# Optimization experiments

Hardware: AMD Instinct MI355X
Metric: run time of the kernel (lower is better)

Reference implementation:

```python
import jax, jax.numpy as jnp
import numpy as np

N = 50000
E = 800000
D = 128
LN_EPS = 1e-5


def setup_inputs() -> dict:
    key = jax.random.key(0)
    ks = jax.random.split(key, 12)
    s = 1.0 / np.sqrt(D)
    return {
        "x": jax.random.normal(ks[0], (N, D), dtype=jnp.float32),
        "edge_index": jax.random.randint(ks[1], (2, E), 0, N, dtype=jnp.int64),
        "edge_attr": jax.random.normal(ks[2], (E, D), dtype=jnp.float32),
        # GINEConv edge projection Linear(edge_dim=D, in_channels=D)
        "Wl": jax.random.uniform(ks[3], (D, D), jnp.float32, -s, s),
        "bl": jax.random.uniform(ks[4], (D,), jnp.float32, -s, s),
        # mlp: Linear(D,D) -> ReLU -> Linear(D,D)
        "W1": jax.random.uniform(ks[5], (D, D), jnp.float32, -s, s),
        "b1": jax.random.uniform(ks[6], (D,), jnp.float32, -s, s),
        "W2": jax.random.uniform(ks[7], (D, D), jnp.float32, -s, s),
        "b2": jax.random.uniform(ks[8], (D,), jnp.float32, -s, s),
        # PyG LayerNorm affine
        "ln_w": jnp.ones((D,), jnp.float32),
        "ln_b": jnp.zeros((D,), jnp.float32),
    }


def reference(x, edge_index, edge_attr, Wl, bl, W1, b1, W2, b2, ln_w, ln_b):
    src = edge_index[0]  # j (message source)
    dst = edge_index[1]  # i (aggregation target)
    # GINEConv message: ReLU(x_j + lin(edge_attr)) -- gather + elementwise
    e = edge_attr @ Wl + bl                      # [E, D]
    msg = jax.nn.relu(x[src] + e)                # [E, D]
    # scatter-sum aggregation into destination nodes
    agg = jax.ops.segment_sum(msg, dst, num_segments=N)  # [N, D]
    # eps = 0 (train_eps=False): nn((1+eps)*x + agg)
    h = x + agg
    h = jax.nn.relu(h @ W1 + b1) @ W2 + b2       # MLP
    # residual
    h = h + x
    # PyG LayerNorm, mode='graph', batch=None: normalize over all entries
    mu = jnp.mean(h)
    std = jnp.sqrt(jnp.mean((h - mu) ** 2))
    h = (h - mu) / (std + LN_EPS) * ln_w + ln_b
    # SiLU, dropout(eval)=identity, nan_to_num
    h = jax.nn.silu(h)
    return jnp.nan_to_num(h)
```

## Files before the change

kernel.cpp:

```cpp
#include <hip/hip_runtime.h>
#include <math.h>

#define NN 50000
#define EE 800000
#define D128 128
#define LN_EPSF 1e-5f

typedef __bf16 bf16_t;
typedef __bf16 bf16x8 __attribute__((ext_vector_type(8)));
typedef float f32x4 __attribute__((ext_vector_type(4)));

#define AGG_F (NN * D128)

__device__ __forceinline__ bf16x8 cvt8(float4 f0, float4 f1) {
    bf16x8 r;
    r[0] = (bf16_t)f0.x; r[1] = (bf16_t)f0.y; r[2] = (bf16_t)f0.z; r[3] = (bf16_t)f0.w;
    r[4] = (bf16_t)f1.x; r[5] = (bf16_t)f1.y; r[6] = (bf16_t)f1.z; r[7] = (bf16_t)f1.w;
    return r;
}

__device__ __forceinline__ bf16x8 zero8() {
    bf16x8 z;
    #pragma unroll
    for (int j = 0; j < 8; ++j) z[j] = (bf16_t)0.f;
    return z;
}

__device__ __forceinline__ void load_w_lds(const float* __restrict__ W, bf16_t* Wlds,
                                           const float* __restrict__ bias, float* b_s) {
    int tid = threadIdx.x;
    for (int i = tid; i < D128 * D128; i += 256) {
        int k = i >> 7, n = i & 127;
        Wlds[(n * D128 + k) ^ ((n & 7) << 3)] = (bf16_t)W[i];
    }
    if (tid < D128) b_s[tid] = bias[tid];
    __syncthreads();
}

__global__ __launch_bounds__(256) void k_zero(float4* __restrict__ agg4,
                                              int* __restrict__ deg,
                                              float* __restrict__ sc) {
    const int idx = blockIdx.x * 256 + threadIdx.x;
    const int stride = gridDim.x * 256;
    const float4 z = {0.f, 0.f, 0.f, 0.f};
    for (int i = idx; i < AGG_F / 4; i += stride) agg4[i] = z;
    for (int i = idx; i < NN; i += stride) deg[i] = 0;
    if (idx == 0) { sc[0] = 0.f; sc[1] = 0.f; }
}

__global__ void k_detect(const int* __restrict__ ei32, int* __restrict__ flag) {
    int i = threadIdx.x;
    unsigned long long m = __ballot(ei32[2 * i + 1] == 0);
    if (i == 0) flag[0] = (m == ~0ULL) ? 1 : 0;
}

__device__ __forceinline__ void idx_pair(const void* ei, int is64, int e, int& sj, int& di) {
    if (is64) {
        const long long* p = (const long long*)ei;
        sj = (int)p[e]; di = (int)p[EE + e];
    } else {
        const int* p = (const int*)ei;
        sj = p[e]; di = p[EE + e];
    }
}


__global__ __launch_bounds__(256) void k_hist(const void* __restrict__ eidx,
                                              const int* __restrict__ flag,
                                              int* __restrict__ deg) {
    const int is64 = flag[0];
    for (int e = blockIdx.x * 256 + threadIdx.x; e < EE; e += gridDim.x * 256) {
        int sj, di;
        idx_pair(eidx, is64, e, sj, di);
        atomicAdd(&deg[di], 1);
    }
}

#define SCAN_T 1024
#define SCAN_SPAN 49
__global__ __launch_bounds__(SCAN_T) void k_scan(const int* __restrict__ deg,
                                                 int* __restrict__ rowptr,
                                                 int* __restrict__ cursor) {
    __shared__ int s[SCAN_T];
    const int t = threadIdx.x;
    const int lo = t * SCAN_SPAN;
    const int hi = min(lo + SCAN_SPAN, NN);
    int part = 0;
    for (int i = lo; i < hi; ++i) part += deg[i];
    s[t] = part;
    __syncthreads();
    #pragma unroll
    for (int off = 1; off < SCAN_T; off <<= 1) {
        int v = (t >= off) ? s[t - off] : 0;
        __syncthreads();
        s[t] += v;
        __syncthreads();
    }
    int run = s[t] - part;
    for (int i = lo; i < hi; ++i) {
        rowptr[i] = run;
        cursor[i] = run;
        run += deg[i];
    }
    if (t == SCAN_T - 1) rowptr[NN] = s[SCAN_T - 1];
}

__global__ __launch_bounds__(256) void k_scatter(const void* __restrict__ eidx,
                                                 const int* __restrict__ flag,
                                                 int* __restrict__ cursor,
                                                 int4* __restrict__ csr4) {
    const int is64 = flag[0];
    for (int e = blockIdx.x * 256 + threadIdx.x; e < EE; e += gridDim.x * 256) {
        int sj, di;
        idx_pair(eidx, is64, e, sj, di);
        int p = atomicAdd(&cursor[di], 1);
        csr4[p] = make_int4(e, sj, di, 0);
    }
}

__global__ __launch_bounds__(256) void k_agg2(
    const float* __restrict__ ea, const float* __restrict__ x,
    const float* __restrict__ Wl, const float* __restrict__ bl,
    const int4* __restrict__ csr4, float* __restrict__ agg)
{
    __shared__ bf16_t Wlds[D128 * D128];
    __shared__ float bl_s[D128];
    __shared__ float msgs[4][16 * 68];
    load_w_lds(Wl, Wlds, bl, bl_s);

    const int lane = threadIdx.x & 63, wid = threadIdx.x >> 6;
    const int l15 = lane & 15, lg = lane >> 4;
    float* msg = msgs[wid];
    const int nwaves = gridDim.x * 4;
    const int NT = EE / 16;

    for (int tile = blockIdx.x * 4 + wid; tile < NT; tile += nwaves) {
        const int p0 = tile * 16;
        const int4 me = csr4[p0 + l15];
        const int eid = me.x, src_l = me.y, dst_l = me.z;
        const int dstm1 = (p0 > 0) ? csr4[p0 - 1].z : -1;
        const int dstp16 = (p0 + 16 < EE) ? csr4[p0 + 16].z : -2;

        bf16x8 a[4];
        {
            const float* rp = ea + (size_t)eid * D128 + lg * 8;
            #pragma unroll
            for (int s = 0; s < 4; ++s) {
                float4 f0 = *(const float4*)(rp + s * 32);
                float4 f1 = *(const float4*)(rp + s * 32 + 4);
                a[s] = cvt8(f0, f1);
            }
        }
        f32x4 acc[8];
        #pragma unroll
        for (int t = 0; t < 8; ++t) acc[t] = f32x4{0.f, 0.f, 0.f, 0.f};
        #pragma unroll
        for (int s = 0; s < 4; ++s) {
            const int kb = s * 32 + lg * 8;
            #pragma unroll
            for (int t = 0; t < 8; ++t) {
                const int col = l15 + 16 * t;
                bf16x8 b = *(const bf16x8*)&Wlds[(col * D128 + kb) ^ ((col & 7) << 3)];
                acc[t] = __builtin_amdgcn_mfma_f32_16x16x32_bf16(a[s], b, acc[t], 0, 0, 0);
            }
        }

        const int prev = __shfl_up(dst_l, 1, 16);
        const bool head = (l15 == 0) || (dst_l != prev);
        const unsigned mask16 = (unsigned)(__ballot(head) & 0xffffu);

        #pragma unroll
        for (int hf = 0; hf < 2; ++hf) {
            #pragma unroll
            for (int i = 0; i < 4; ++i) {
                const int r = lg * 4 + i;
                const int src_r = __shfl(src_l, r, 16);
                const float* xr = x + (size_t)src_r * D128 + hf * 64;
                #pragma unroll
                for (int t = 0; t < 4; ++t) {
                    const int cl = l15 + 16 * t;
                    float v = fmaxf(acc[hf * 4 + t][i] + bl_s[hf * 64 + cl] + xr[cl], 0.f);
                    msg[r * 68 + cl] = v;
                }
            }
            asm volatile("s_waitcnt lgkmcnt(0)" ::: "memory");
            unsigned m = mask16;
            while (m) {
                const int h = __builtin_ctz(m);
                m &= m - 1;
                const int nxt = m ? __builtin_ctz(m) : 16;
                const int dst_run = __shfl(dst_l, h, 16);
                float s = 0.f;
                for (int r = h; r < nxt; ++r) s += msg[r * 68 + lane];
                const bool part = (h == 0 && dst_run == dstm1) ||
                                  (nxt == 16 && dst_run == dstp16);
                float* ap = agg + (size_t)dst_run * D128 + hf * 64 + lane;
                if (part) unsafeAtomicAdd(ap, s);
                else *ap = s;
            }
            asm volatile("s_waitcnt lgkmcnt(0)" ::: "memory");
        }
    }
}

__global__ __launch_bounds__(256) void k_mlp1(
    const float* __restrict__ x, const float* __restrict__ agg,
    const float* __restrict__ W1, const float* __restrict__ b1,
    float* __restrict__ tbuf)
{
    __shared__ bf16_t Wlds[D128 * D128];
    __shared__ float b_s[D128];
    load_w_lds(W1, Wlds, b1, b_s);

    const int lane = threadIdx.x & 63, wid = threadIdx.x >> 6;
    const int l15 = lane & 15, lg = lane >> 4;
    const int nbase = blockIdx.x * 64 + wid * 16;
    if (nbase >= NN) return;

    const int row = nbase + l15;
    bf16x8 a[4];
    if (row < NN) {
        const float* xr = x + (size_t)row * D128 + lg * 8;
        const float* gr = agg + (size_t)row * D128 + lg * 8;
        #pragma unroll
        for (int s = 0; s < 4; ++s) {
            float4 f0 = *(const float4*)(xr + s * 32);
            float4 f1 = *(const float4*)(xr + s * 32 + 4);
            float4 g0 = *(const float4*)(gr + s * 32);
            float4 g1 = *(const float4*)(gr + s * 32 + 4);
            float4 h0 = {f0.x + g0.x, f0.y + g0.y, f0.z + g0.z, f0.w + g0.w};
            float4 h1 = {f1.x + g1.x, f1.y + g1.y, f1.z + g1.z, f1.w + g1.w};
            a[s] = cvt8(h0, h1);
        }
    } else {
        #pragma unroll
        for (int s = 0; s < 4; ++s) a[s] = zero8();
    }
    f32x4 acc[8];
    #pragma unroll
    for (int t = 0; t < 8; ++t) acc[t] = f32x4{0.f, 0.f, 0.f, 0.f};
    #pragma unroll
    for (int s = 0; s < 4; ++s) {
        const int kb = s * 32 + lg * 8;
        #pragma unroll
        for (int t = 0; t < 8; ++t) {
            const int col = l15 + 16 * t;
            bf16x8 b = *(const bf16x8*)&Wlds[(col * D128 + kb) ^ ((col & 7) << 3)];
            acc[t] = __builtin_amdgcn_mfma_f32_16x16x32_bf16(a[s], b, acc[t], 0, 0, 0);
        }
    }
    #pragma unroll
    for (int i = 0; i < 4; ++i) {
        const int r = nbase + lg * 4 + i;
        if (r < NN) {
            float* tr = tbuf + (size_t)r * D128;
            #pragma unroll
            for (int t = 0; t < 8; ++t) {
                const int c = l15 + 16 * t;
                tr[c] = fmaxf(acc[t][i] + b_s[c], 0.0f);
            }
        }
    }
}

__global__ __launch_bounds__(256) void k_mlp2(
    const float* __restrict__ tbuf, const float* __restrict__ x,
    const float* __restrict__ W2, const float* __restrict__ b2,
    float* __restrict__ out, float* __restrict__ sc)
{
    __shared__ bf16_t Wlds[D128 * D128];
    __shared__ float b_s[D128];
    __shared__ float red[8];
    load_w_lds(W2, Wlds, b2, b_s);

    const int tid = threadIdx.x;
    const int lane = tid & 63, wid = tid >> 6;
    const int l15 = lane & 15, lg = lane >> 4;
    const int nbase = blockIdx.x * 64 + wid * 16;
    float s1 = 0.f, s2 = 0.f;

    if (nbase < NN) {
        const int row = nbase + l15;
        bf16x8 a[4];
        if (row < NN) {
            const float* rp = tbuf + (size_t)row * D128 + lg * 8;
            #pragma unroll
            for (int s = 0; s < 4; ++s) {
                float4 f0 = *(const float4*)(rp + s * 32);
                float4 f1 = *(const float4*)(rp + s * 32 + 4);
                a[s] = cvt8(f0, f1);
            }
        } else {
            #pragma unroll
            for (int s = 0; s < 4; ++s) a[s] = zero8();
        }
        f32x4 acc[8];
        #pragma unroll
        for (int t = 0; t < 8; ++t) acc[t] = f32x4{0.f, 0.f, 0.f, 0.f};
        #pragma unroll
        for (int s = 0; s < 4; ++s) {
            const int kb = s * 32 + lg * 8;
            #pragma unroll
            for (int t = 0; t < 8; ++t) {
                const int col = l15 + 16 * t;
                bf16x8 b = *(const bf16x8*)&Wlds[(col * D128 + kb) ^ ((col & 7) << 3)];
                acc[t] = __builtin_amdgcn_mfma_f32_16x16x32_bf16(a[s], b, acc[t], 0, 0, 0);
            }
        }
        #pragma unroll
        for (int i = 0; i < 4; ++i) {
            const int r = nbase + lg * 4 + i;
            if (r < NN) {
                #pragma unroll
                for (int t = 0; t < 8; ++t) {
                    const int c = l15 + 16 * t;
                    float v = acc[t][i] + b_s[c] + x[(size_t)r * D128 + c];
                    out[(size_t)r * D128 + c] = v;
                    s1 += v;
                    s2 += v * v;
                }
            }
        }
    }
    #pragma unroll
    for (int o = 32; o > 0; o >>= 1) {
        s1 += __shfl_xor(s1, o);
        s2 += __shfl_xor(s2, o);
    }
    if (lane == 0) { red[wid * 2] = s1; red[wid * 2 + 1] = s2; }
    __syncthreads();
    if (tid == 0) {
        float a1 = red[0] + red[2] + red[4] + red[6];
        float a2 = red[1] + red[3] + red[5] + red[7];
        unsafeAtomicAdd(&sc[0], a1);
        unsafeAtomicAdd(&sc[1], a2);
    }
}

__global__ __launch_bounds__(256) void k_ln(
    float* __restrict__ out, const float* __restrict__ sc,
    const float* __restrict__ lnw, const float* __restrict__ lnb)
{
    const float inv = 1.0f / (float)(NN * D128);
    const float mu = sc[0] * inv;
    const float var = sc[1] * inv - mu * mu;
    const float rstd = 1.0f / (sqrtf(fmaxf(var, 0.f)) + LN_EPSF);
    const int total = NN * D128 / 4;
    for (int idx = blockIdx.x * 256 + threadIdx.x; idx < total; idx += gridDim.x * 256) {
        float4 h = ((const float4*)out)[idx];
        const int c0 = (idx * 4) & 127;
        float4 w = *(const float4*)(lnw + c0);
        float4 bb = *(const float4*)(lnb + c0);
        float4 r;
        r.x = (h.x - mu) * rstd * w.x + bb.x;
        r.y = (h.y - mu) * rstd * w.y + bb.y;
        r.z = (h.z - mu) * rstd * w.z + bb.z;
        r.w = (h.w - mu) * rstd * w.w + bb.w;
        r.x = r.x / (1.f + __expf(-r.x));
        r.y = r.y / (1.f + __expf(-r.y));
        r.z = r.z / (1.f + __expf(-r.z));
        r.w = r.w / (1.f + __expf(-r.w));
        if (r.x != r.x) r.x = 0.f;
        if (r.y != r.y) r.y = 0.f;
        if (r.z != r.z) r.z = 0.f;
        if (r.w != r.w) r.w = 0.f;
        ((float4*)out)[idx] = r;
    }
}

extern "C" void kernel_launch(void* const* d_in, const int* in_sizes, int n_in,
                              void* d_out, int out_size, void* d_ws, size_t ws_size,
                              hipStream_t stream)
{
    const float* x   = (const float*)d_in[0];
    const void*  ei  = d_in[1];
    const float* ea  = (const float*)d_in[2];
    const float* Wl  = (const float*)d_in[3];
    const float* bl  = (const float*)d_in[4];
    const float* W1  = (const float*)d_in[5];
    const float* b1  = (const float*)d_in[6];
    const float* W2  = (const float*)d_in[7];
    const float* b2  = (const float*)d_in[8];
    const float* lnw = (const float*)d_in[9];
    const float* lnb = (const float*)d_in[10];
    float* out = (float*)d_out;

    float* agg = (float*)d_ws;
    float* sc  = agg + AGG_F;
    int* flag  = (int*)(sc + 2);

    int4* csr4  = (int4*)d_out;
    int* deg    = (int*)(csr4 + EE);
    int* rowptr = deg + NN;
    int* cursor = rowptr + NN + 1;

    k_zero<<<2048, 256, 0, stream>>>((float4*)agg, deg, sc);
    k_detect<<<1, 64, 0, stream>>>((const int*)ei, flag);
    k_hist<<<1024, 256, 0, stream>>>(ei, flag, deg);
    k_scan<<<1, SCAN_T, 0, stream>>>(deg, rowptr, cursor);
    k_scatter<<<1024, 256, 0, stream>>>(ei, flag, cursor, csr4);
    k_agg2<<<768, 256, 0, stream>>>(ea, x, Wl, bl, csr4, agg);
    k_mlp1<<<(NN + 63) / 64, 256, 0, stream>>>(x, agg, W1, b1, out);
    k_mlp2<<<(NN + 63) / 64, 256, 0, stream>>>(out, x, W2, b2, out, sc);
    k_ln<<<NN * D128 / 4 / 256, 256, 0, stream>>>(out, sc, lnw, lnb);
}
```

Before: 415.3 us.

## Rewrite edge aggregation with contiguous tile ranges, prefetch, and register-side segment reduction

The edge aggregation kernel now gives each wave a contiguous range of tiles and software-pipelines the loop. It prefetches the next tile's edge_attr rows and CSR entries while computing the current one. The gathered x rows are added into the accumulators through an identity-matrix MFMA in bf16, and the per-destination segment sums are reduced in registers with cross-lane shuffles instead of an LDS message buffer. Contiguous ranges let the previous tile's last destination carry over in a register, and the grid grows to 1024 blocks. In exchange, x now enters the sum at bf16 precision, register pressure rises, and the per-run reduction does more shuffle work.

After: 442.6 us. 1.07x slower.

```diff
diff --git a/kernel.cpp b/kernel.cpp
--- a/kernel.cpp
+++ b/kernel.cpp
@@ -118,88 +118,146 @@
     }
 }
 
-__global__ __launch_bounds__(256) void k_agg2(
+__global__ __launch_bounds__(256) void k_agg3(
     const float* __restrict__ ea, const float* __restrict__ x,
     const float* __restrict__ Wl, const float* __restrict__ bl,
     const int4* __restrict__ csr4, float* __restrict__ agg)
 {
     __shared__ bf16_t Wlds[D128 * D128];
     __shared__ float bl_s[D128];
-    __shared__ float msgs[4][16 * 68];
     load_w_lds(Wl, Wlds, bl, bl_s);
 
     const int lane = threadIdx.x & 63, wid = threadIdx.x >> 6;
     const int l15 = lane & 15, lg = lane >> 4;
-    float* msg = msgs[wid];
-    const int nwaves = gridDim.x * 4;
+
+    bf16x8 id0 = zero8(), id1 = zero8();
+    #pragma unroll
+    for (int j = 0; j < 8; ++j) {
+        if (8 * lg + j == l15)      id0[j] = (bf16_t)1.0f;
+        if (8 * lg + j == l15 + 16) id1[j] = (bf16_t)1.0f;
+    }
+    float blv[8];
+    #pragma unroll
+    for (int t = 0; t < 8; ++t) blv[t] = bl_s[l15 + 16 * t];
+
     const int NT = EE / 16;
-
-    for (int tile = blockIdx.x * 4 + wid; tile < NT; tile += nwaves) {
-        const int p0 = tile * 16;
-        const int4 me = csr4[p0 + l15];
-        const int eid = me.x, src_l = me.y, dst_l = me.z;
-        const int dstm1 = (p0 > 0) ? csr4[p0 - 1].z : -1;
-        const int dstp16 = (p0 + 16 < EE) ? csr4[p0 + 16].z : -2;
-
-        bf16x8 a[4];
+    const int waves = gridDim.x * 4;
+    const int wgid = blockIdx.x * 4 + wid;
+    const int TPW = (NT + waves - 1) / waves;
+    const int t0 = wgid * TPW;
+    const int t1 = min(t0 + TPW, NT);
+    if (t0 >= t1) return;
+
+    int4 meC = csr4[(size_t)t0 * 16 + l15];
+    int dstm1 = (t0 > 0) ? csr4[(size_t)t0 * 16 - 1].z : -1;
+    int4 meN = (t0 + 1 < NT) ? csr4[(size_t)(t0 + 1) * 16 + l15]
+                             : make_int4(0, 0, -2, 0);
+    float4 cA[8];
+    {
+        const float* rp = ea + (size_t)meC.x * D128 + lg * 8;
+        #pragma unroll
+        for (int s = 0; s < 4; ++s) {
+            cA[2 * s]     = *(const float4*)(rp + s * 32);
+            cA[2 * s + 1] = *(const float4*)(rp + s * 32 + 4);
+        }
+    }
+
+    for (int t = t0; t < t1; ++t) {
+        const bool nic = (t + 1) < t1;
+        const bool ne  = (t + 1) < NT;
+
+        float4 xR[8];
         {
-            const float* rp = ea + (size_t)eid * D128 + lg * 8;
+            const float* rp = x + (size_t)meC.y * D128 + lg * 8;
             #pragma unroll
             for (int s = 0; s < 4; ++s) {
-                float4 f0 = *(const float4*)(rp + s * 32);
-                float4 f1 = *(const float4*)(rp + s * 32 + 4);
-                a[s] = cvt8(f0, f1);
-            }
-        }
+                xR[2 * s]     = *(const float4*)(rp + s * 32);
+                xR[2 * s + 1] = *(const float4*)(rp + s * 32 + 4);
+            }
+        }
+        float4 nA[8];
+        if (nic) {
+            const float* rp = ea + (size_t)meN.x * D128 + lg * 8;
+            #pragma unroll
+            for (int s = 0; s < 4; ++s) {
+                nA[2 * s]     = *(const float4*)(rp + s * 32);
+                nA[2 * s + 1] = *(const float4*)(rp + s * 32 + 4);
+            }
+        }
+        int4 meNN = make_int4(0, 0, -2, 0);
+        if (t + 2 < NT) meNN = csr4[(size_t)(t + 2) * 16 + l15];
+
         f32x4 acc[8];
         #pragma unroll
-        for (int t = 0; t < 8; ++t) acc[t] = f32x4{0.f, 0.f, 0.f, 0.f};
+        for (int q = 0; q < 8; ++q) acc[q] = f32x4{0.f, 0.f, 0.f, 0.f};
         #pragma unroll
         for (int s = 0; s < 4; ++s) {
+            const bf16x8 af = cvt8(cA[2 * s], cA[2 * s + 1]);
             const int kb = s * 32 + lg * 8;
             #pragma unroll
-            for (int t = 0; t < 8; ++t) {
-                const int col = l15 + 16 * t;
+            for (int q = 0; q < 8; ++q) {
+                const int col = l15 + 16 * q;
                 bf16x8 b = *(const bf16x8*)&Wlds[(col * D128 + kb) ^ ((col & 7) << 3)];
-                acc[t] = __builtin_amdgcn_mfma_f32_16x16x32_bf16(a[s], b, acc[t], 0, 0, 0);
-            }
-        }
-
+                acc[q] = __builtin_amdgcn_mfma_f32_16x16x32_bf16(af, b, acc[q], 0, 0, 0);
+            }
+        }
+        #pragma unroll
+        for (int s = 0; s < 4; ++s) {
+            const bf16x8 xf = cvt8(xR[2 * s], xR[2 * s + 1]);
+            acc[2 * s]     = __builtin_amdgcn_mfma_f32_16x16x32_bf16(xf, id0, acc[2 * s], 0, 0, 0);
+            acc[2 * s + 1] = __builtin_amdgcn_mfma_f32_16x16x32_bf16(xf, id1, acc[2 * s + 1], 0, 0, 0);
+        }
+        #pragma unroll
+        for (int q = 0; q < 8; ++q)
+            #pragma unroll
+            for (int i = 0; i < 4; ++i)
+                acc[q][i] = fmaxf(acc[q][i] + blv[q], 0.f);
+
+        const int dst_l = meC.z;
         const int prev = __shfl_up(dst_l, 1, 16);
         const bool head = (l15 == 0) || (dst_l != prev);
-        const unsigned mask16 = (unsigned)(__ballot(head) & 0xffffu);
-
-        #pragma unroll
-        for (int hf = 0; hf < 2; ++hf) {
+        unsigned m = (unsigned)(__ballot(head) & 0xffffu);
+        const int dstp16 = ne ? __shfl(meN.z, 0, 16) : -2;
+
+        while (m) {
+            const int h = __builtin_ctz(m);
+            m &= m - 1;
+            const int nxt = m ? __builtin_ctz(m) : 16;
+            const int dst_run = __shfl(dst_l, h, 16);
+            float sv[8];
+            #pragma unroll
+            for (int q = 0; q < 8; ++q) sv[q] = 0.f;
             #pragma unroll
             for (int i = 0; i < 4; ++i) {
                 const int r = lg * 4 + i;
-                const int src_r = __shfl(src_l, r, 16);
-                const float* xr = x + (size_t)src_r * D128 + hf * 64;
+                const bool in = (r >= h) && (r < nxt);
                 #pragma unroll
-                for (int t = 0; t < 4; ++t) {
-                    const int cl = l15 + 16 * t;
-                    float v = fmaxf(acc[hf * 4 + t][i] + bl_s[hf * 64 + cl] + xr[cl], 0.f);
-                    msg[r * 68 + cl] = v;
+                for (int q = 0; q < 8; ++q) sv[q] += in ? acc[q][i] : 0.f;
+            }
+            #pragma unroll
+            for (int q = 0; q < 8; ++q) {
+                sv[q] += __shfl_xor(sv[q], 16);
+                sv[q] += __shfl_xor(sv[q], 32);
+            }
+            const bool part = (h == 0 && dst_run == dstm1) ||
+                              (nxt == 16 && dst_run == dstp16);
+            if (lg == 0) {
+                float* ap = agg + (size_t)dst_run * D128 + l15;
+                if (part) {
+                    #pragma unroll
+                    for (int q = 0; q < 8; ++q) unsafeAtomicAdd(ap + 16 * q, sv[q]);
+                } else {
+                    #pragma unroll
+                    for (int q = 0; q < 8; ++q) ap[16 * q] = sv[q];
                 }
             }
-            asm volatile("s_waitcnt lgkmcnt(0)" ::: "memory");
-            unsigned m = mask16;
-            while (m) {
-                const int h = __builtin_ctz(m);
-                m &= m - 1;
-                const int nxt = m ? __builtin_ctz(m) : 16;
-                const int dst_run = __shfl(dst_l, h, 16);
-                float s = 0.f;
-                for (int r = h; r < nxt; ++r) s += msg[r * 68 + lane];
-                const bool part = (h == 0 && dst_run == dstm1) ||
-                                  (nxt == 16 && dst_run == dstp16);
-                float* ap = agg + (size_t)dst_run * D128 + hf * 64 + lane;
-                if (part) unsafeAtomicAdd(ap, s);
-                else *ap = s;
-            }
-            asm volatile("s_waitcnt lgkmcnt(0)" ::: "memory");
-        }
+        }
+
+        dstm1 = __shfl(dst_l, 15, 16);
+        meC = meN;
+        meN = meNN;
+        #pragma unroll
+        for (int k = 0; k < 8; ++k) cA[k] = nA[k];
     }
 }
 
@@ -399,7 +457,7 @@
     k_hist<<<1024, 256, 0, stream>>>(ei, flag, deg);
     k_scan<<<1, SCAN_T, 0, stream>>>(deg, rowptr, cursor);
     k_scatter<<<1024, 256, 0, stream>>>(ei, flag, cursor, csr4);
-    k_agg2<<<768, 256, 0, stream>>>(ea, x, Wl, bl, csr4, agg);
+    k_agg3<<<1024, 256, 0, stream>>>(ea, x, Wl, bl, csr4, agg);
     k_mlp1<<<(NN + 63) / 64, 256, 0, stream>>>(x, agg, W1, b1, out);
     k_mlp2<<<(NN + 63) / 64, 256, 0, stream>>>(out, x, W2, b2, out, sc);
     k_ln<<<NN * D128 / 4 / 256, 256, 0, stream>>>(out, sc, lnw, lnb);
```

## Fold x gather into MFMA via identity matrix and launch one tile per wave

Applied to the files above, without the earlier changes.

The source-node row of x is now loaded as coalesced float4 vectors alongside edge_attr, converted to bf16, and added into the accumulators through extra MFMAs against an identity B operand. This replaces the per-element scalar x loads in the epilogue. The grid grows from 768 to 12500 blocks, so each wave handles a single tile. The aim is better latency hiding and cheaper x access, but every block now reloads Wl into LDS, and x is rounded to bf16 before the add, which lowers accuracy.

After: 502.1 us. +20.9%, slower.

```diff
diff --git a/kernel.cpp b/kernel.cpp
--- a/kernel.cpp
+++ b/kernel.cpp
@@ -134,35 +134,54 @@
     const int nwaves = gridDim.x * 4;
     const int NT = EE / 16;
 
-    for (int tile = blockIdx.x * 4 + wid; tile < NT; tile += nwaves) {
-        const int p0 = tile * 16;
+    bf16x8 id0 = zero8(), id1 = zero8();
+    #pragma unroll
+    for (int j = 0; j < 8; ++j) {
+        if (8 * lg + j == l15)      id0[j] = (bf16_t)1.0f;
+        if (8 * lg + j == l15 + 16) id1[j] = (bf16_t)1.0f;
+    }
+
+    for (int tile = blockIdx.x; tile < NT; tile += gridDim.x * 4 / 4 * 0 + nwaves / 4 * 0 + gridDim.x) {
+        const int t = tile * 4 + wid;
+        if (t >= NT) continue;
+        const int p0 = t * 16;
         const int4 me = csr4[p0 + l15];
         const int eid = me.x, src_l = me.y, dst_l = me.z;
         const int dstm1 = (p0 > 0) ? csr4[p0 - 1].z : -1;
         const int dstp16 = (p0 + 16 < EE) ? csr4[p0 + 16].z : -2;
 
-        bf16x8 a[4];
+        float4 eA[8], xA[8];
         {
             const float* rp = ea + (size_t)eid * D128 + lg * 8;
             #pragma unroll
             for (int s = 0; s < 4; ++s) {
-                float4 f0 = *(const float4*)(rp + s * 32);
-                float4 f1 = *(const float4*)(rp + s * 32 + 4);
-                a[s] = cvt8(f0, f1);
-            }
-        }
+                eA[2 * s]     = *(const float4*)(rp + s * 32);
+                eA[2 * s + 1] = *(const float4*)(rp + s * 32 + 4);
+            }
+            const float* xp = x + (size_t)src_l * D128 + lg * 8;
+            #pragma unroll
+            for (int s = 0; s < 4; ++s) {
+                xA[2 * s]     = *(const float4*)(xp + s * 32);
+                xA[2 * s + 1] = *(const float4*)(xp + s * 32 + 4);
+            }
+        }
+
         f32x4 acc[8];
         #pragma unroll
-        for (int t = 0; t < 8; ++t) acc[t] = f32x4{0.f, 0.f, 0.f, 0.f};
+        for (int q = 0; q < 8; ++q) acc[q] = f32x4{0.f, 0.f, 0.f, 0.f};
         #pragma unroll
         for (int s = 0; s < 4; ++s) {
+            const bf16x8 af = cvt8(eA[2 * s], eA[2 * s + 1]);
             const int kb = s * 32 + lg * 8;
             #pragma unroll
-            for (int t = 0; t < 8; ++t) {
-                const int col = l15 + 16 * t;
+            for (int q = 0; q < 8; ++q) {
+                const int col = l15 + 16 * q;
                 bf16x8 b = *(const bf16x8*)&Wlds[(col * D128 + kb) ^ ((col & 7) << 3)];
-                acc[t] = __builtin_amdgcn_mfma_f32_16x16x32_bf16(a[s], b, acc[t], 0, 0, 0);
-            }
+                acc[q] = __builtin_amdgcn_mfma_f32_16x16x32_bf16(af, b, acc[q], 0, 0, 0);
+            }
+            const bf16x8 xf = cvt8(xA[2 * s], xA[2 * s + 1]);
+            acc[2 * s]     = __builtin_amdgcn_mfma_f32_16x16x32_bf16(xf, id0, acc[2 * s], 0, 0, 0);
+            acc[2 * s + 1] = __builtin_amdgcn_mfma_f32_16x16x32_bf16(xf, id1, acc[2 * s + 1], 0, 0, 0);
         }
 
         const int prev = __shfl_up(dst_l, 1, 16);
@@ -174,12 +193,10 @@
             #pragma unroll
             for (int i = 0; i < 4; ++i) {
                 const int r = lg * 4 + i;
-                const int src_r = __shfl(src_l, r, 16);
-                const float* xr = x + (size_t)src_r * D128 + hf * 64;
                 #pragma unroll
-                for (int t = 0; t < 4; ++t) {
-                    const int cl = l15 + 16 * t;
-                    float v = fmaxf(acc[hf * 4 + t][i] + bl_s[hf * 64 + cl] + xr[cl], 0.f);
+                for (int q = 0; q < 4; ++q) {
+                    const int cl = l15 + 16 * q;
+                    float v = fmaxf(acc[hf * 4 + q][i] + bl_s[hf * 64 + cl], 0.f);
                     msg[r * 68 + cl] = v;
                 }
             }
@@ -399,7 +416,7 @@
     k_hist<<<1024, 256, 0, stream>>>(ei, flag, deg);
     k_scan<<<1, SCAN_T, 0, stream>>>(deg, rowptr, cursor);
     k_scatter<<<1024, 256, 0, stream>>>(ei, flag, cursor, csr4);
-    k_agg2<<<768, 256, 0, stream>>>(ea, x, Wl, bl, csr4, agg);
+    k_agg2<<<12500, 256, 0, stream>>>(ea, x, Wl, bl, csr4, agg);
     k_mlp1<<<(NN + 63) / 64, 256, 0, stream>>>(x, agg, W1, b1, out);
     k_mlp2<<<(NN + 63) / 64, 256, 0, stream>>>(out, x, W2, b2, out, sc);
     k_ln<<<NN * D128 / 4 / 256, 256, 0, stream>>>(out, sc, lnw, lnb);
```
